# Kernel optimization log

Hardware: AMD Instinct MI355X
Metric: run time of the kernel (lower is better)

## Reference

```python
import jax, jax.numpy as jnp
import numpy as np

B, IN, H = 4096, 1024, 1024


def setup_inputs() -> dict:
    key = jax.random.key(0)
    ks = jax.random.split(key, 6)
    s_h = 1.0 / np.sqrt(H)
    s_x = 1.0 / np.sqrt(IN)
    return {
        "x": jax.random.normal(ks[0], (B, IN), jnp.float32),
        "h": jax.random.normal(ks[1], (B, H), jnp.float32),
        "c": jax.random.normal(ks[2], (B, H), jnp.float32),
        # hidden_lin: Linear(H, 4H) with bias
        "Wh": jax.random.uniform(ks[3], (4 * H, H), jnp.float32, -s_h, s_h),
        "bh": jax.random.uniform(ks[4], (4 * H,), jnp.float32, -s_h, s_h),
        # input_lin: Linear(IN, 4H), bias=False
        "Wx": jax.random.uniform(ks[5], (4 * H, IN), jnp.float32, -s_x, s_x),
    }


def reference(x, h, c, Wh, bh, Wx):
    # ifgo = h @ Wh^T + bh + x @ Wx^T   -> [B, 4H]
    ifgo = jnp.dot(h, Wh.T) + bh + jnp.dot(x, Wx.T)
    i, f, g, o = jnp.split(ifgo, 4, axis=1)
    i = jax.nn.sigmoid(i)
    f = jax.nn.sigmoid(f)
    g = jnp.tanh(g)
    o = jax.nn.sigmoid(o)
    c_next = f * c + i * g
    h_next = o * jnp.tanh(c_next)
    return (h_next, c_next)
```

## Files before the change

kernel.cpp:

```cpp
#include <hip/hip_runtime.h>
#include <cstdint>
#include <cstddef>


#define NB   4096
#define KH   1024
#define NOUT 4096
#define ARR_ELEMS 4194304

typedef __bf16 bf16x8 __attribute__((ext_vector_type(8)));
typedef float  f32x4  __attribute__((ext_vector_type(4)));

__device__ inline unsigned short f2bf(float f) {
    union { float f; unsigned int u; } v; v.f = f;
    unsigned int u = v.u;
    u += 0x7FFFu + ((u >> 16) & 1u);
    return (unsigned short)(u >> 16);
}
__device__ inline float bf2f(unsigned short s) {
    union { unsigned int u; float f; } v; v.u = ((unsigned int)s) << 16;
    return v.f;
}

__global__ void convert_kernel(const float* __restrict__ h, const float* __restrict__ x,
                               const float* __restrict__ Wh, const float* __restrict__ Wx,
                               unsigned short* __restrict__ dst) {
    int idx = blockIdx.x * 256 + threadIdx.x;
    int arr = idx >> 20;
    int off = (idx & 0xFFFFF) << 2;
    const float* src = (arr == 0) ? h : (arr == 1) ? x : (arr == 2) ? Wh : Wx;
    float4 v = *(const float4*)(src + off);
    unsigned int lo = (unsigned int)f2bf(v.x) | ((unsigned int)f2bf(v.y) << 16);
    unsigned int hi = (unsigned int)f2bf(v.z) | ((unsigned int)f2bf(v.w) << 16);
    uint2 packed; packed.x = lo; packed.y = hi;
    *(uint2*)(dst + (size_t)arr * ARR_ELEMS + off) = packed;
}

__global__ void gemm_kernel(const unsigned short* __restrict__ Ah,
                            const unsigned short* __restrict__ Ax,
                            const unsigned short* __restrict__ Bh,
                            const unsigned short* __restrict__ Bx,
                            unsigned short* __restrict__ C) {
    __shared__ __align__(16) unsigned short As[128 * 32];
    __shared__ __align__(16) unsigned short Bs[128 * 32];

    const int tid  = threadIdx.x;
    const int wave = tid >> 6;
    const int lane = tid & 63;
    const int tileN = blockIdx.x;
    const int tileM = blockIdx.y;

    const int stRow  = wave * 16 + (lane >> 2);
    const int stColE = (lane & 3) * 8;
    const size_t gaRow = (size_t)(tileM * 128 + stRow) * KH;
    const size_t gbRow = (size_t)(tileN * 128 + stRow) * KH;

    const int mBase = (wave >> 1) * 64;
    const int nBase = (wave & 1) * 64;
    const int fr = lane & 15;
    const int fk = (lane >> 4) * 8;

    f32x4 acc[4][4] = {};

    for (int kt = 0; kt < 64; ++kt) {
        const unsigned short* Aseg = (kt < 32) ? Ah : Ax;
        const unsigned short* Bseg = (kt < 32) ? Bh : Bx;
        const int kk = (kt & 31) * 32;

        const unsigned short* ga0 = Aseg + gaRow + kk + stColE;
        const unsigned short* gb0 = Bseg + gbRow + kk + stColE;
        __builtin_amdgcn_global_load_lds(
            (const __attribute__((address_space(1))) void*)ga0,
            (__attribute__((address_space(3))) void*)(As + wave * 512), 16, 0, 0);
        __builtin_amdgcn_global_load_lds(
            (const __attribute__((address_space(1))) void*)(ga0 + 64 * KH),
            (__attribute__((address_space(3))) void*)(As + 2048 + wave * 512), 16, 0, 0);
        __builtin_amdgcn_global_load_lds(
            (const __attribute__((address_space(1))) void*)gb0,
            (__attribute__((address_space(3))) void*)(Bs + wave * 512), 16, 0, 0);
        __builtin_amdgcn_global_load_lds(
            (const __attribute__((address_space(1))) void*)(gb0 + 64 * KH),
            (__attribute__((address_space(3))) void*)(Bs + 2048 + wave * 512), 16, 0, 0);

        __syncthreads();

        bf16x8 a[4], b[4];
        #pragma unroll
        for (int i = 0; i < 4; ++i)
            a[i] = *(const bf16x8*)(As + (mBase + i * 16 + fr) * 32 + fk);
        #pragma unroll
        for (int j = 0; j < 4; ++j)
            b[j] = *(const bf16x8*)(Bs + (nBase + j * 16 + fr) * 32 + fk);

        #pragma unroll
        for (int i = 0; i < 4; ++i)
            #pragma unroll
            for (int j = 0; j < 4; ++j)
                acc[i][j] = __builtin_amdgcn_mfma_f32_16x16x32_bf16(a[i], b[j], acc[i][j], 0, 0, 0);

        __syncthreads();
    }

    const int col0 = tileN * 128 + nBase + (lane & 15);
    const int row0 = tileM * 128 + mBase + (lane >> 4) * 4;
    #pragma unroll
    for (int i = 0; i < 4; ++i)
        #pragma unroll
        for (int j = 0; j < 4; ++j)
            #pragma unroll
            for (int r = 0; r < 4; ++r)
                C[(size_t)(row0 + i * 16 + r) * NOUT + (col0 + j * 16)] = f2bf(acc[i][j][r]);
}

__global__ void lstm_epilogue(const unsigned short* __restrict__ ifgo,
                              const float* __restrict__ bh,
                              const float* __restrict__ c,
                              float* __restrict__ out) {
    int tid = blockIdx.x * 256 + threadIdx.x;
    int b = tid >> 10, j = tid & 1023;
    const unsigned short* row = ifgo + (size_t)b * NOUT;
    float iv = bf2f(row[j])        + bh[j];
    float fv = bf2f(row[j + 1024]) + bh[j + 1024];
    float gv = bf2f(row[j + 2048]) + bh[j + 2048];
    float ov = bf2f(row[j + 3072]) + bh[j + 3072];
    iv = 1.f / (1.f + __expf(-iv));
    fv = 1.f / (1.f + __expf(-fv));
    ov = 1.f / (1.f + __expf(-ov));
    gv = tanhf(gv);
    float cn = fv * c[tid] + iv * gv;
    float hn = ov * tanhf(cn);
    out[tid] = hn;
    out[ARR_ELEMS + tid] = cn;
}

extern "C" void kernel_launch(void* const* d_in, const int* in_sizes, int n_in,
                              void* d_out, int out_size, void* d_ws, size_t ws_size,
                              hipStream_t stream) {
    const float* x  = (const float*)d_in[0];
    const float* h  = (const float*)d_in[1];
    const float* c  = (const float*)d_in[2];
    const float* Wh = (const float*)d_in[3];
    const float* bh = (const float*)d_in[4];
    const float* Wx = (const float*)d_in[5];
    float* out = (float*)d_out;

    unsigned short* ws   = (unsigned short*)d_ws;
    unsigned short* Ahb  = ws;
    unsigned short* Axb  = ws + 1 * (size_t)ARR_ELEMS;
    unsigned short* Whb  = ws + 2 * (size_t)ARR_ELEMS;
    unsigned short* Wxb  = ws + 3 * (size_t)ARR_ELEMS;
    unsigned short* ifgo = ws + 4 * (size_t)ARR_ELEMS;

    convert_kernel<<<16384, 256, 0, stream>>>(h, x, Wh, Wx, ws);
    dim3 grid(NOUT / 128, NB / 128);
    gemm_kernel<<<grid, 256, 0, stream>>>(Ahb, Axb, Whb, Wxb, ifgo);
    lstm_epilogue<<<16384, 256, 0, stream>>>(ifgo, bh, c, out);
}
```

Baseline: 223.0 us.

## Fuse LSTM gate epilogue into GEMM via gate-interleaved weight row permutation

Weight rows are permuted during bf16 conversion so that each 64-column output tile holds the i, f, g and o gates for the same 16 hidden units. That lets the GEMM apply bias, the gate activations and the cell update directly from accumulators. This removes the bf16 ifgo intermediate round-trip through memory and the separate epilogue kernel launch. The cost is a scattered write pattern in the conversion kernel and epilogue stores in the GEMM that are only 16 floats contiguous per row.

```diff
diff --git a/kernel.cpp b/kernel.cpp
--- a/kernel.cpp
+++ b/kernel.cpp
@@ -17,10 +17,8 @@
     u += 0x7FFFu + ((u >> 16) & 1u);
     return (unsigned short)(u >> 16);
 }
-__device__ inline float bf2f(unsigned short s) {
-    union { unsigned int u; float f; } v; v.u = ((unsigned int)s) << 16;
-    return v.f;
-}
+
+__device__ inline float sigmoidf(float v) { return 1.f / (1.f + __expf(-v)); }
 
 __global__ void convert_kernel(const float* __restrict__ h, const float* __restrict__ x,
                                const float* __restrict__ Wh, const float* __restrict__ Wx,
@@ -33,14 +31,25 @@
     unsigned int lo = (unsigned int)f2bf(v.x) | ((unsigned int)f2bf(v.y) << 16);
     unsigned int hi = (unsigned int)f2bf(v.z) | ((unsigned int)f2bf(v.w) << 16);
     uint2 packed; packed.x = lo; packed.y = hi;
-    *(uint2*)(dst + (size_t)arr * ARR_ELEMS + off) = packed;
+
+    int dstOff = off;
+    if (arr >= 2) {
+        int L   = off >> 10;
+        int col = off & 1023;
+        int g = L >> 10, j = L & 1023;
+        int p = ((j >> 4) << 6) | (g << 4) | (j & 15);
+        dstOff = (p << 10) | col;
+    }
+    *(uint2*)(dst + (size_t)arr * ARR_ELEMS + dstOff) = packed;
 }
 
 __global__ void gemm_kernel(const unsigned short* __restrict__ Ah,
                             const unsigned short* __restrict__ Ax,
                             const unsigned short* __restrict__ Bh,
                             const unsigned short* __restrict__ Bx,
-                            unsigned short* __restrict__ C) {
+                            const float* __restrict__ bh,
+                            const float* __restrict__ c,
+                            float* __restrict__ out) {
     __shared__ __align__(16) unsigned short As[128 * 32];
     __shared__ __align__(16) unsigned short Bs[128 * 32];
 
@@ -101,36 +110,29 @@
         __syncthreads();
     }
 
-    const int col0 = tileN * 128 + nBase + (lane & 15);
+    const int j = ((tileN * 2 + (wave & 1)) << 4) | (lane & 15);
+    const float bi = bh[j];
+    const float bf = bh[j + 1024];
+    const float bg = bh[j + 2048];
+    const float bo = bh[j + 3072];
+
     const int row0 = tileM * 128 + mBase + (lane >> 4) * 4;
     #pragma unroll
-    for (int i = 0; i < 4; ++i)
+    for (int i = 0; i < 4; ++i) {
         #pragma unroll
-        for (int j = 0; j < 4; ++j)
-            #pragma unroll
-            for (int r = 0; r < 4; ++r)
-                C[(size_t)(row0 + i * 16 + r) * NOUT + (col0 + j * 16)] = f2bf(acc[i][j][r]);
-}
-
-__global__ void lstm_epilogue(const unsigned short* __restrict__ ifgo,
-                              const float* __restrict__ bh,
-                              const float* __restrict__ c,
-                              float* __restrict__ out) {
-    int tid = blockIdx.x * 256 + threadIdx.x;
-    int b = tid >> 10, j = tid & 1023;
-    const unsigned short* row = ifgo + (size_t)b * NOUT;
-    float iv = bf2f(row[j])        + bh[j];
-    float fv = bf2f(row[j + 1024]) + bh[j + 1024];
-    float gv = bf2f(row[j + 2048]) + bh[j + 2048];
-    float ov = bf2f(row[j + 3072]) + bh[j + 3072];
-    iv = 1.f / (1.f + __expf(-iv));
-    fv = 1.f / (1.f + __expf(-fv));
-    ov = 1.f / (1.f + __expf(-ov));
-    gv = tanhf(gv);
-    float cn = fv * c[tid] + iv * gv;
-    float hn = ov * tanhf(cn);
-    out[tid] = hn;
-    out[ARR_ELEMS + tid] = cn;
+        for (int r = 0; r < 4; ++r) {
+            const int m = row0 + i * 16 + r;
+            const size_t idx = (size_t)m * KH + j;
+            float iv = sigmoidf(acc[i][0][r] + bi);
+            float fv = sigmoidf(acc[i][1][r] + bf);
+            float gv = tanhf(acc[i][2][r] + bg);
+            float ov = sigmoidf(acc[i][3][r] + bo);
+            float cn = fv * c[idx] + iv * gv;
+            float hn = ov * tanhf(cn);
+            out[idx] = hn;
+            out[(size_t)ARR_ELEMS + idx] = cn;
+        }
+    }
 }
 
 extern "C" void kernel_launch(void* const* d_in, const int* in_sizes, int n_in,
@@ -144,15 +146,13 @@
     const float* Wx = (const float*)d_in[5];
     float* out = (float*)d_out;
 
-    unsigned short* ws   = (unsigned short*)d_ws;
-    unsigned short* Ahb  = ws;
-    unsigned short* Axb  = ws + 1 * (size_t)ARR_ELEMS;
-    unsigned short* Whb  = ws + 2 * (size_t)ARR_ELEMS;
-    unsigned short* Wxb  = ws + 3 * (size_t)ARR_ELEMS;
-    unsigned short* ifgo = ws + 4 * (size_t)ARR_ELEMS;
+    unsigned short* ws  = (unsigned short*)d_ws;
+    unsigned short* Ahb = ws;
+    unsigned short* Axb = ws + 1 * (size_t)ARR_ELEMS;
+    unsigned short* Whb = ws + 2 * (size_t)ARR_ELEMS;
+    unsigned short* Wxb = ws + 3 * (size_t)ARR_ELEMS;
 
     convert_kernel<<<16384, 256, 0, stream>>>(h, x, Wh, Wx, ws);
     dim3 grid(NOUT / 128, NB / 128);
-    gemm_kernel<<<grid, 256, 0, stream>>>(Ahb, Axb, Whb, Wxb, ifgo);
-    lstm_epilogue<<<16384, 256, 0, stream>>>(ifgo, bh, c, out);
+    gemm_kernel<<<grid, 256, 0, stream>>>(Ahb, Axb, Whb, Wxb, bh, c, out);
 }
```

Result: faster. 216.6 us (-2.8%).
